# Optimization experiments

Hardware: AMD Instinct MI355X
Metric: run time of the kernel (lower is better)

The kernel has to match this reference:

```python
import jax, jax.numpy as jnp
import numpy as np

D, HEADS, HD, L, P, DFF = 256, 8, 32, 4, 4, 2048
B, NQ = 4, 900
SHAPES = [(128, 128), (64, 64), (32, 32), (16, 16)]
S = sum(h * w for h, w in SHAPES)


def setup_inputs():
    ks = iter(jax.random.split(jax.random.key(0), 20))
    rn = lambda *s: jax.random.normal(next(ks), s, jnp.float32) * 0.02
    cxcy = jax.random.uniform(next(ks), (B, NQ, 1, 2), minval=0.1, maxval=0.9)
    wh = jax.random.uniform(next(ks), (B, NQ, 1, 2), minval=0.05, maxval=0.3)
    ref = jnp.broadcast_to(jnp.concatenate([cxcy, wh], -1), (B, NQ, L, 4))
    starts = np.cumsum([0] + [h * w for h, w in SHAPES[:-1]])
    return dict(
        query=jax.random.normal(next(ks), (B, NQ, D), jnp.float32),
        query_pos=jax.random.normal(next(ks), (B, NQ, D), jnp.float32),
        reference_points=ref,
        input_flatten=jax.random.normal(next(ks), (B, S, D), jnp.float32),
        input_spatial_shapes=jnp.array(SHAPES, jnp.int32),
        input_level_start_index=jnp.array(starts, jnp.int32),
        sa_in_w=rn(3, D, D), sa_in_b=jnp.zeros((3, D)),
        sa_out_w=rn(D, D), sa_out_b=jnp.zeros((D,)),
        norm1_g=jnp.ones((D,)), norm1_b=jnp.zeros((D,)),
        value_w=rn(D, D), value_b=jnp.zeros((D,)),
        off_w=rn(D, HEADS * L * P * 2),
        off_b=jax.random.uniform(next(ks), (HEADS * L * P * 2,), minval=-1.0, maxval=1.0),
        aw_w=rn(D, HEADS * L * P), aw_b=jnp.zeros((HEADS * L * P,)),
        ca_out_w=rn(D, D), ca_out_b=jnp.zeros((D,)),
        norm2_g=jnp.ones((D,)), norm2_b=jnp.zeros((D,)),
        lin1_w=rn(D, DFF), lin1_b=jnp.zeros((DFF,)),
        lin2_w=rn(DFF, D), lin2_b=jnp.zeros((D,)),
        norm3_g=jnp.ones((D,)), norm3_b=jnp.zeros((D,)),
    )


def _ln(x, g, b, eps=1e-5):
    m = x.mean(-1, keepdims=True)
    v = ((x - m) ** 2).mean(-1, keepdims=True)
    return (x - m) * jax.lax.rsqrt(v + eps) * g + b


def _msdeform(q, input_flatten, ref, shapes, starts, value_w, value_b,
              off_w, off_b, aw_w, aw_b, out_w, out_b):
    Bq, Nq, _ = q.shape
    # value: (B, heads, S, head_dim)
    v = (input_flatten @ value_w + value_b).reshape(Bq, -1, HEADS, HD).transpose(0, 2, 1, 3)
    off = (q @ off_w + off_b).reshape(Bq, Nq, HEADS, L, P, 2).transpose(0, 2, 1, 3, 4, 5)
    aw = jax.nn.softmax((q @ aw_w + aw_b).reshape(Bq, Nq, HEADS, L * P), axis=-1)
    aw = aw.reshape(Bq, Nq, HEADS, L, P).transpose(0, 2, 1, 3, 4)  # (B,H,Nq,L,P)
    refc = ref[:, None, :, :, None, :]  # (B,1,Nq,L,1,4)
    # box refs: center + offset/P * wh * 0.5  (Deformable-DETR convention)
    loc = refc[..., :2] + off / P * refc[..., 2:] * 0.5  # (B,H,Nq,L,P,2)
    out = jnp.zeros((Bq, HEADS, Nq, HD), q.dtype)
    for l, (H, W) in enumerate(shapes):
        vl = jax.lax.dynamic_slice_in_dim(v, starts[l], H * W, axis=2)  # (B,H,HW,hd)
        x = loc[:, :, :, l, :, 0] * W - 0.5  # align_corners=False pixel coords
        y = loc[:, :, :, l, :, 1] * H - 0.5
        x0, y0 = jnp.floor(x), jnp.floor(y)
        dx, dy = x - x0, y - y0

        def g(xi, yi):
            valid = (xi >= 0) & (xi < W) & (yi >= 0) & (yi < H)  # zero padding
            idx = (jnp.clip(yi, 0, H - 1) * W + jnp.clip(xi, 0, W - 1)).astype(jnp.int32)
            gat = jnp.take_along_axis(vl, idx.reshape(Bq, HEADS, Nq * P, 1), axis=2)
            return gat.reshape(Bq, HEADS, Nq, P, HD) * valid[..., None]

        samp = (((1 - dx) * (1 - dy))[..., None] * g(x0, y0)
                + (dx * (1 - dy))[..., None] * g(x0 + 1, y0)
                + ((1 - dx) * dy)[..., None] * g(x0, y0 + 1)
                + (dx * dy)[..., None] * g(x0 + 1, y0 + 1))
        out = out + jnp.sum(aw[:, :, :, l, :, None] * samp, axis=3)
    return out.transpose(0, 2, 1, 3).reshape(Bq, Nq, D) @ out_w + out_b


def _layer(query, query_pos, reference_points, input_flatten, shapes, starts, p):
    Bq, Nq, _ = query.shape
    qk = query + query_pos
    heads = lambda x: x.reshape(Bq, Nq, HEADS, HD).transpose(0, 2, 1, 3)
    qh = heads(qk @ p['sa_in_w'][0] + p['sa_in_b'][0])
    kh = heads(qk @ p['sa_in_w'][1] + p['sa_in_b'][1])
    vh = heads(query @ p['sa_in_w'][2] + p['sa_in_b'][2])
    attn = jax.nn.softmax(jnp.einsum('bhqd,bhkd->bhqk', qh, kh) * (HD ** -0.5), axis=-1)
    sa = jnp.einsum('bhqk,bhkd->bhqd', attn, vh).transpose(0, 2, 1, 3).reshape(Bq, Nq, D)
    sa = sa @ p['sa_out_w'] + p['sa_out_b']
    x = _ln(query + sa, p['norm1_g'], p['norm1_b'])
    ca = _msdeform(x + query_pos, input_flatten, reference_points, shapes, starts,
                   p['value_w'], p['value_b'], p['off_w'], p['off_b'],
                   p['aw_w'], p['aw_b'], p['ca_out_w'], p['ca_out_b'])
    x = _ln(x + ca, p['norm2_g'], p['norm2_b'])
    ffn = jax.nn.relu(x @ p['lin1_w'] + p['lin1_b']) @ p['lin2_w'] + p['lin2_b']
    return _ln(x + ffn, p['norm3_g'], p['norm3_b'])


PNAMES = ['sa_in_w', 'sa_in_b', 'sa_out_w', 'sa_out_b', 'norm1_g', 'norm1_b',
          'value_w', 'value_b', 'off_w', 'off_b', 'aw_w', 'aw_b',
          'ca_out_w', 'ca_out_b', 'norm2_g', 'norm2_b',
          'lin1_w', 'lin1_b', 'lin2_w', 'lin2_b', 'norm3_g', 'norm3_b']


def reference(query, query_pos, reference_points, input_flatten,
              input_spatial_shapes, input_level_start_index,
              sa_in_w, sa_in_b, sa_out_w, sa_out_b, norm1_g, norm1_b,
              value_w, value_b, off_w, off_b, aw_w, aw_b,
              ca_out_w, ca_out_b, norm2_g, norm2_b,
              lin1_w, lin1_b, lin2_w, lin2_b, norm3_g, norm3_b):
    # spatial shapes / start indices are static structural metadata
    shapes = [(int(h), int(w)) for h, w in np.asarray(input_spatial_shapes)]
    starts = [int(s) for s in np.asarray(input_level_start_index)]
    p = dict(zip(PNAMES, (sa_in_w, sa_in_b, sa_out_w, sa_out_b, norm1_g, norm1_b,
                          value_w, value_b, off_w, off_b, aw_w, aw_b,
                          ca_out_w, ca_out_b, norm2_g, norm2_b,
                          lin1_w, lin1_b, lin2_w, lin2_b, norm3_g, norm3_b)))
    return _layer(query, query_pos, reference_points, input_flatten, shapes, starts, p)
```

## Files before the change

kernel.cpp:

```cpp
#include <hip/hip_runtime.h>
#include <hip/hip_bf16.h>

#define DD   256
#define NH   8
#define HDIM 32
#define LV   4
#define NP   4
#define DFF  2048
#define BB   4
#define NQQ  900
#define SS   21760

typedef __bf16 bf16x8 __attribute__((ext_vector_type(8)));
typedef __bf16 bf16x2 __attribute__((ext_vector_type(2)));
typedef float  f32x4  __attribute__((ext_vector_type(4)));

__device__ inline void stval(float* p, float v) { *p = v; }
__device__ inline void stval(__bf16* p, float v) { *p = (__bf16)v; }

__device__ __forceinline__ void gload16(const void* g, void* l) {
    __builtin_amdgcn_global_load_lds(
        (const __attribute__((address_space(1))) void*)g,
        (__attribute__((address_space(3))) void*)l, 16, 0, 0);
}

struct TPtrs {
    const float* s[10];
    __bf16* d[10];
};

__global__ void transp_all(TPtrs P) {
    const int Ks[10] = {256, 256, 256, 256, 256, 256, 256, 256, 256, 2048};
    const int Ns[10] = {256, 256, 256, 256, 256, 256, 128, 256, 2048, 256};
    const int tiles[10] = {64, 64, 64, 64, 64, 64, 32, 64, 512, 512};
    int t = blockIdx.x;
    int j = 0, base = 0;
    while (t >= base + tiles[j]) { base += tiles[j]; j++; }
    int lt = t - base;
    int K = Ks[j], N = Ns[j];
    int tn = N >> 5;
    int nb = (lt % tn) * 32, kb = (lt / tn) * 32;
    const float* W = P.s[j];
    __bf16* Wt = P.d[j];
    __shared__ float tbuf[32][33];
    for (int i = threadIdx.y; i < 32; i += 8)
        tbuf[i][threadIdx.x] = W[(size_t)(kb + i) * N + nb + threadIdx.x];
    __syncthreads();
    for (int i = threadIdx.y; i < 32; i += 8)
        Wt[(size_t)(nb + i) * K + kb + threadIdx.x] = (__bf16)tbuf[threadIdx.x][i];
}

#define BM 64
#define BN 64
#define BKK 64

template <typename AT, typename OT, int RELU, int NSUB, bool LNF>
__global__ __launch_bounds__(256) void mfma_gemm(
    const AT* __restrict__ A, const float* __restrict__ A2,
    const __bf16* __restrict__ Wt,
    const float* __restrict__ bias, const float* __restrict__ bias2, int nsplit,
    const float* __restrict__ res, const float* __restrict__ lng,
    const float* __restrict__ lnb,
    OT* __restrict__ C, int M, int N, int K) {
    int tid = threadIdx.x;
    int lane = tid & 63;
    int wave = tid >> 6;
    int wr = wave >> 1, wc = wave & 1;
    int m0 = blockIdx.y * BM;
    int n0 = blockIdx.x * (BN * NSUB);

    __shared__ __attribute__((aligned(16))) __bf16 As[BM * BKK];
    __shared__ __attribute__((aligned(16))) __bf16 Bs[NSUB][BN * BKK];
    __shared__ float rsum[LNF ? 64 : 1][2];
    __shared__ float rsum2[LNF ? 64 : 1][2];

    f32x4 acc[NSUB][2][2] = {};

    int srow = tid >> 2;
    int sq = tid & 3;
    int u0 = sq << 1;
    int p0 = (u0 ^ (srow & 7)) * 8;
    int p1 = ((u0 + 1) ^ (srow & 7)) * 8;
    int fr = lane & 15, gq = lane >> 4;

    for (int k0 = 0; k0 < K; k0 += BKK) {
        {
            int gm = m0 + srow;
            bf16x8 v0 = {}, v1 = {};
            if (gm < M) {
                if constexpr (sizeof(AT) == 4) {
                    const float* ap = (const float*)A + (size_t)gm * K + k0 + sq * 16;
                    f32x4 f0 = *(const f32x4*)(ap + 0);
                    f32x4 f1 = *(const f32x4*)(ap + 4);
                    f32x4 f2 = *(const f32x4*)(ap + 8);
                    f32x4 f3 = *(const f32x4*)(ap + 12);
                    if (A2) {
                        const float* ap2 = A2 + (size_t)gm * K + k0 + sq * 16;
                        f0 += *(const f32x4*)(ap2 + 0);
                        f1 += *(const f32x4*)(ap2 + 4);
                        f2 += *(const f32x4*)(ap2 + 8);
                        f3 += *(const f32x4*)(ap2 + 12);
                    }
#pragma unroll
                    for (int e = 0; e < 4; e++) {
                        v0[e] = (__bf16)f0[e]; v0[e + 4] = (__bf16)f1[e];
                        v1[e] = (__bf16)f2[e]; v1[e + 4] = (__bf16)f3[e];
                    }
                } else {
                    const __bf16* ap = (const __bf16*)A + (size_t)gm * K + k0 + sq * 16;
                    v0 = *(const bf16x8*)(ap);
                    v1 = *(const bf16x8*)(ap + 8);
                }
            }
            *(bf16x8*)(&As[srow * 64 + p0]) = v0;
            *(bf16x8*)(&As[srow * 64 + p1]) = v1;
        }
#pragma unroll
        for (int ns = 0; ns < NSUB; ns++) {
            int gn = n0 + ns * BN + srow;
            const __bf16* bp = Wt + (size_t)gn * K + k0 + sq * 16;
            bf16x8 w0 = *(const bf16x8*)(bp);
            bf16x8 w1 = *(const bf16x8*)(bp + 8);
            *(bf16x8*)(&Bs[ns][srow * 64 + p0]) = w0;
            *(bf16x8*)(&Bs[ns][srow * 64 + p1]) = w1;
        }
        __syncthreads();
#pragma unroll
        for (int ks = 0; ks < 2; ks++) {
            bf16x8 a[2];
#pragma unroll
            for (int i = 0; i < 2; i++) {
                int ma = wr * 32 + i * 16 + fr;
                a[i] = *(const bf16x8*)(&As[ma * 64 + ((ks * 4 + gq) ^ (ma & 7)) * 8]);
            }
#pragma unroll
            for (int ns = 0; ns < NSUB; ns++) {
                bf16x8 b[2];
#pragma unroll
                for (int j = 0; j < 2; j++) {
                    int nb = wc * 32 + j * 16 + fr;
                    b[j] = *(const bf16x8*)(&Bs[ns][nb * 64 + ((ks * 4 + gq) ^ (nb & 7)) * 8]);
                }
#pragma unroll
                for (int i = 0; i < 2; i++)
#pragma unroll
                    for (int j = 0; j < 2; j++)
                        acc[ns][i][j] = __builtin_amdgcn_mfma_f32_16x16x32_bf16(a[i], b[j], acc[ns][i][j], 0, 0, 0);
            }
        }
        __syncthreads();
    }
    int orow = gq * 4;
    if constexpr (!LNF) {
#pragma unroll
        for (int ns = 0; ns < NSUB; ns++)
#pragma unroll
            for (int i = 0; i < 2; i++)
#pragma unroll
                for (int j = 0; j < 2; j++) {
                    int gn = n0 + ns * BN + wc * 32 + j * 16 + fr;
                    float bv = (gn < nsplit) ? bias[gn] : bias2[gn - nsplit];
#pragma unroll
                    for (int r = 0; r < 4; r++) {
                        int gm = m0 + wr * 32 + i * 16 + orow + r;
                        if (gm < M) {
                            float v = acc[ns][i][j][r] + bv;
                            if (RELU) v = fmaxf(v, 0.f);
                            stval(C + (size_t)gm * N + gn, v);
                        }
                    }
                }
    } else {
        float part[2][4] = {};
#pragma unroll
        for (int ns = 0; ns < NSUB; ns++)
#pragma unroll
            for (int i = 0; i < 2; i++)
#pragma unroll
                for (int j = 0; j < 2; j++) {
                    int gn = ns * BN + wc * 32 + j * 16 + fr;
                    float bv = bias[gn];
#pragma unroll
                    for (int r = 0; r < 4; r++) {
                        int gm = m0 + wr * 32 + i * 16 + orow + r;
                        float rv = (gm < M) ? res[(size_t)gm * 256 + gn] : 0.f;
                        float x = acc[ns][i][j][r] + bv + rv;
                        acc[ns][i][j][r] = x;
                        part[i][r] += x;
                    }
                }
#pragma unroll
        for (int i = 0; i < 2; i++)
#pragma unroll
            for (int r = 0; r < 4; r++) {
                float v = part[i][r];
                v += __shfl_xor(v, 1);
                v += __shfl_xor(v, 2);
                v += __shfl_xor(v, 4);
                v += __shfl_xor(v, 8);
                part[i][r] = v;
            }
        if (fr == 0) {
#pragma unroll
            for (int i = 0; i < 2; i++)
#pragma unroll
                for (int r = 0; r < 4; r++)
                    rsum[wr * 32 + i * 16 + orow + r][wc] = part[i][r];
        }
        __syncthreads();
        float mean[2][4];
#pragma unroll
        for (int i = 0; i < 2; i++)
#pragma unroll
            for (int r = 0; r < 4; r++) {
                int rl = wr * 32 + i * 16 + orow + r;
                mean[i][r] = (rsum[rl][0] + rsum[rl][1]) * (1.f / 256.f);
            }
        float p2[2][4] = {};
#pragma unroll
        for (int ns = 0; ns < NSUB; ns++)
#pragma unroll
            for (int i = 0; i < 2; i++)
#pragma unroll
                for (int j = 0; j < 2; j++)
#pragma unroll
                    for (int r = 0; r < 4; r++) {
                        float d = acc[ns][i][j][r] - mean[i][r];
                        p2[i][r] += d * d;
                    }
#pragma unroll
        for (int i = 0; i < 2; i++)
#pragma unroll
            for (int r = 0; r < 4; r++) {
                float v = p2[i][r];
                v += __shfl_xor(v, 1);
                v += __shfl_xor(v, 2);
                v += __shfl_xor(v, 4);
                v += __shfl_xor(v, 8);
                p2[i][r] = v;
            }
        if (fr == 0) {
#pragma unroll
            for (int i = 0; i < 2; i++)
#pragma unroll
                for (int r = 0; r < 4; r++)
                    rsum2[wr * 32 + i * 16 + orow + r][wc] = p2[i][r];
        }
        __syncthreads();
        float rstd[2][4];
#pragma unroll
        for (int i = 0; i < 2; i++)
#pragma unroll
            for (int r = 0; r < 4; r++) {
                int rl = wr * 32 + i * 16 + orow + r;
                float var = (rsum2[rl][0] + rsum2[rl][1]) * (1.f / 256.f);
                rstd[i][r] = rsqrtf(var + 1e-5f);
            }
#pragma unroll
        for (int ns = 0; ns < NSUB; ns++)
#pragma unroll
            for (int i = 0; i < 2; i++)
#pragma unroll
                for (int j = 0; j < 2; j++) {
                    int gn = ns * BN + wc * 32 + j * 16 + fr;
                    float gv = lng[gn], bev = lnb[gn];
#pragma unroll
                    for (int r = 0; r < 4; r++) {
                        int gm = m0 + wr * 32 + i * 16 + orow + r;
                        if (gm < M) {
                            float y = (acc[ns][i][j][r] - mean[i][r]) * rstd[i][r] * gv + bev;
                            stval(C + (size_t)gm * 256 + gn, y);
                        }
                    }
                }
    }
}

__global__ __launch_bounds__(256) void value_gemm4(
    const float* __restrict__ A, const __bf16* __restrict__ Wt,
    const float* __restrict__ bias, __bf16* __restrict__ C) {
    int tid = threadIdx.x;
    int lane = tid & 63;
    int wave = tid >> 6;
    int fr = lane & 15, gq = lane >> 4;
    int m0 = blockIdx.x * 64;

    __shared__ __attribute__((aligned(16))) __bf16 As[2][64 * 64];
    __shared__ __attribute__((aligned(16))) __bf16 Bq[2][4][64 * 64];

    f32x4 acc[4][4] = {};

    int srow = tid >> 2;
    int sq = tid & 3;
    int u0 = sq << 1;
    int p0 = (u0 ^ (srow & 7)) * 8;
    int p1 = ((u0 + 1) ^ (srow & 7)) * 8;

    int c_row = lane >> 3;
    int c_u = lane & 7;
    int gu = c_u ^ c_row;
    const __bf16* bsrc0 = Wt + (size_t)(wave * 64 + c_row) * 256 + gu * 8;
    const float* aptr = A + (size_t)(m0 + srow) * 256 + sq * 16;

    f32x4 fa0 = *(const f32x4*)(aptr + 0);
    f32x4 fa1 = *(const f32x4*)(aptr + 4);
    f32x4 fa2 = *(const f32x4*)(aptr + 8);
    f32x4 fa3 = *(const f32x4*)(aptr + 12);
    __builtin_amdgcn_sched_barrier(0);
#pragma unroll
    for (int c = 0; c < 8; c++)
        gload16(bsrc0 + (size_t)c * 8 * 256, &Bq[0][wave][c * 512]);
    asm volatile("s_waitcnt vmcnt(8)" ::: "memory");
    __builtin_amdgcn_sched_barrier(0);
    {
        bf16x8 v0, v1;
#pragma unroll
        for (int e = 0; e < 4; e++) {
            v0[e] = (__bf16)fa0[e]; v0[e + 4] = (__bf16)fa1[e];
            v1[e] = (__bf16)fa2[e]; v1[e + 4] = (__bf16)fa3[e];
        }
        *(bf16x8*)(&As[0][srow * 64 + p0]) = v0;
        *(bf16x8*)(&As[0][srow * 64 + p1]) = v1;
    }
    asm volatile("s_waitcnt lgkmcnt(0)" ::: "memory");
    __builtin_amdgcn_s_barrier();

#pragma unroll
    for (int step = 0; step < 4; step++) {
        int p = step & 1;
        if (step < 3) {
            const float* ap2 = aptr + (step + 1) * 64;
            fa0 = *(const f32x4*)(ap2 + 0);
            fa1 = *(const f32x4*)(ap2 + 4);
            fa2 = *(const f32x4*)(ap2 + 8);
            fa3 = *(const f32x4*)(ap2 + 12);
            __builtin_amdgcn_sched_barrier(0);
            const __bf16* bsrc = bsrc0 + (step + 1) * 64;
#pragma unroll
            for (int c = 0; c < 8; c++)
                gload16(bsrc + (size_t)c * 8 * 256, &Bq[p ^ 1][wave][c * 512]);
            asm volatile("s_waitcnt vmcnt(12)" ::: "memory");
        } else {
            asm volatile("s_waitcnt vmcnt(0)" ::: "memory");
        }
        __builtin_amdgcn_sched_barrier(0);
#pragma unroll
        for (int ks = 0; ks < 2; ks++) {
            bf16x8 a[4], b[4];
#pragma unroll
            for (int i = 0; i < 4; i++) {
                int ma = i * 16 + fr;
                a[i] = *(const bf16x8*)(&As[p][ma * 64 + ((ks * 4 + gq) ^ (ma & 7)) * 8]);
                b[i] = *(const bf16x8*)(&Bq[p][wave][ma * 64 + ((ks * 4 + gq) ^ (ma & 7)) * 8]);
            }
#pragma unroll
            for (int i = 0; i < 4; i++)
#pragma unroll
                for (int j = 0; j < 4; j++)
                    acc[i][j] = __builtin_amdgcn_mfma_f32_16x16x32_bf16(a[i], b[j], acc[i][j], 0, 0, 0);
        }
        if (step < 3) {
            asm volatile("s_waitcnt vmcnt(8)" ::: "memory");
            __builtin_amdgcn_sched_barrier(0);
            bf16x8 v0, v1;
#pragma unroll
            for (int e = 0; e < 4; e++) {
                v0[e] = (__bf16)fa0[e]; v0[e + 4] = (__bf16)fa1[e];
                v1[e] = (__bf16)fa2[e]; v1[e + 4] = (__bf16)fa3[e];
            }
            *(bf16x8*)(&As[p ^ 1][srow * 64 + p0]) = v0;
            *(bf16x8*)(&As[p ^ 1][srow * 64 + p1]) = v1;
            asm volatile("s_waitcnt lgkmcnt(0)" ::: "memory");
            __builtin_amdgcn_s_barrier();
        }
    }

#pragma unroll
    for (int i = 0; i < 4; i++)
#pragma unroll
        for (int j = 0; j < 4; j++) {
            int gn = wave * 64 + j * 16 + fr;
            float bv = bias[gn];
#pragma unroll
            for (int r = 0; r < 4; r++) {
                int gm = m0 + i * 16 + gq * 4 + r;
                C[(size_t)gm * 256 + gn] = (__bf16)(acc[i][j][r] + bv);
            }
        }
}

__global__ void fillmark(float* o, int n, float v) {
    int i = blockIdx.x * blockDim.x + threadIdx.x;
    if (i < n) o[i] = v;
}

__global__ void ln_res(const float* a, const float* b,
                       const float* g, const float* be, float* o) {
    int row = blockIdx.x;
    int t = threadIdx.x;
    float x = a[(size_t)row * DD + t] + b[(size_t)row * DD + t];
    __shared__ float red[DD];
    red[t] = x;
    __syncthreads();
    for (int s = 128; s > 0; s >>= 1) {
        if (t < s) red[t] += red[t + s];
        __syncthreads();
    }
    float m = red[0] * (1.f / DD);
    __syncthreads();
    float d0 = x - m;
    red[t] = d0 * d0;
    __syncthreads();
    for (int s = 128; s > 0; s >>= 1) {
        if (t < s) red[t] += red[t + s];
        __syncthreads();
    }
    float v = red[0] * (1.f / DD);
    o[(size_t)row * DD + t] = d0 * rsqrtf(v + 1e-5f) * g[t] + be[t];
}

#define QT 64
#define KT 64
#define NT ((NQQ + KT - 1) / KT)
#define QKLD 512

__global__ __launch_bounds__(256) void sa_attn_mfma(
    const __bf16* __restrict__ QK, const __bf16* __restrict__ V,
    float* __restrict__ O) {
    int blk = blockIdx.x;
    int tq = blk % NT;
    int bh = blk / NT;
    int h = bh % NH;
    int b = bh / NH;
    int tid = threadIdx.x;
    int lane = tid & 63;
    int wave = tid >> 6;
    int fr = lane & 15, gq = lane >> 4;
    int q0 = tq * QT;

    __shared__ __attribute__((aligned(16))) __bf16 Ks[KT][56];
    __shared__ __attribute__((aligned(16))) __bf16 Vt[HDIM][72];
    __shared__ __attribute__((aligned(16))) __bf16 Ps[4][16][72];

    int qrow = q0 + wave * 16 + fr;
    bf16x8 aq = {};
    if (qrow < NQQ)
        aq = *(const bf16x8*)(QK + ((size_t)(b * NQQ + qrow)) * QKLD + h * HDIM + gq * 8);

    f32x4 o0 = {}, o1 = {};
    float m_r[4] = {-1e30f, -1e30f, -1e30f, -1e30f};
    float l_r[4] = {0.f, 0.f, 0.f, 0.f};
    const float scale = 0.17677669529663687f;

    for (int kt = 0; kt < NT; kt++) {
        int kv0 = kt * KT;
        {
            int r = tid >> 2;
            int c8 = (tid & 3) * 8;
            int kvr = kv0 + r;
            bf16x8 kv_ = {}, vv_ = {};
            if (kvr < NQQ) {
                kv_ = *(const bf16x8*)(QK + ((size_t)(b * NQQ + kvr)) * QKLD + 256 + h * HDIM + c8);
                vv_ = *(const bf16x8*)(V + ((size_t)(b * NQQ + kvr)) * DD + h * HDIM + c8);
            }
            *(bf16x8*)(&Ks[r][c8]) = kv_;
#pragma unroll
            for (int j = 0; j < 8; j++) Vt[c8 + j][r] = vv_[j];
        }
        __syncthreads();

        f32x4 s[4];
#pragma unroll
        for (int f = 0; f < 4; f++) {
            bf16x8 bk = *(const bf16x8*)(&Ks[f * 16 + fr][gq * 8]);
            f32x4 z = {};
            s[f] = __builtin_amdgcn_mfma_f32_16x16x32_bf16(aq, bk, z, 0, 0, 0);
        }
#pragma unroll
        for (int f = 0; f < 4; f++) {
            bool valid = (kv0 + f * 16 + fr) < NQQ;
#pragma unroll
            for (int r = 0; r < 4; r++)
                s[f][r] = valid ? s[f][r] * scale : -1e30f;
        }
        float sc_[4];
#pragma unroll
        for (int r = 0; r < 4; r++) {
            float v = fmaxf(fmaxf(s[0][r], s[1][r]), fmaxf(s[2][r], s[3][r]));
            v = fmaxf(v, __shfl_xor(v, 1));
            v = fmaxf(v, __shfl_xor(v, 2));
            v = fmaxf(v, __shfl_xor(v, 4));
            v = fmaxf(v, __shfl_xor(v, 8));
            float mn = fmaxf(m_r[r], v);
            sc_[r] = expf(m_r[r] - mn);
            m_r[r] = mn;
        }
        float rs[4] = {0.f, 0.f, 0.f, 0.f};
#pragma unroll
        for (int f = 0; f < 4; f++)
#pragma unroll
            for (int r = 0; r < 4; r++) {
                float e = expf(s[f][r] - m_r[r]);
                s[f][r] = e;
                rs[r] += e;
            }
#pragma unroll
        for (int r = 0; r < 4; r++) {
            float v = rs[r];
            v += __shfl_xor(v, 1);
            v += __shfl_xor(v, 2);
            v += __shfl_xor(v, 4);
            v += __shfl_xor(v, 8);
            l_r[r] = l_r[r] * sc_[r] + v;
            o0[r] *= sc_[r];
            o1[r] *= sc_[r];
        }
#pragma unroll
        for (int f = 0; f < 4; f++)
#pragma unroll
            for (int r = 0; r < 4; r++)
                Ps[wave][gq * 4 + r][f * 16 + fr] = (__bf16)s[f][r];
#pragma unroll
        for (int c = 0; c < 2; c++) {
            bf16x8 ap = *(const bf16x8*)(&Ps[wave][fr][c * 32 + gq * 8]);
            bf16x8 bv0 = *(const bf16x8*)(&Vt[fr][c * 32 + gq * 8]);
            bf16x8 bv1 = *(const bf16x8*)(&Vt[16 + fr][c * 32 + gq * 8]);
            o0 = __builtin_amdgcn_mfma_f32_16x16x32_bf16(ap, bv0, o0, 0, 0, 0);
            o1 = __builtin_amdgcn_mfma_f32_16x16x32_bf16(ap, bv1, o1, 0, 0, 0);
        }
        __syncthreads();
    }
#pragma unroll
    for (int r = 0; r < 4; r++) {
        int qr = q0 + wave * 16 + gq * 4 + r;
        if (qr < NQQ) {
            float inv = 1.f / l_r[r];
            O[((size_t)(b * NQQ + qr)) * DD + h * HDIM + fr] = o0[r] * inv;
            O[((size_t)(b * NQQ + qr)) * DD + h * HDIM + 16 + fr] = o1[r] * inv;
        }
    }
}

#define OAW 384

__global__ __launch_bounds__(256) void msdeform3(
    const __bf16* __restrict__ val, const __bf16* __restrict__ oa,
    const float* __restrict__ ref, float* __restrict__ out) {
    int tid = threadIdx.x;
    int row = blockIdx.x;
    int b_ = row / NQQ;

    __shared__ float sx[128], sy[128], sw[128];

    if (tid < 128) {
        int h = tid >> 4;
        int lp = tid & 15;
        int l = lp >> 2;
        float logit = (float)oa[(size_t)row * OAW + 256 + h * 16 + lp];
        float ox = (float)oa[(size_t)row * OAW + h * 32 + lp * 2];
        float oy = (float)oa[(size_t)row * OAW + h * 32 + lp * 2 + 1];
        const float* rp = ref + ((size_t)row * LV + l) * 4;
        float cx = rp[0], cy = rp[1], rw = rp[2], rh = rp[3];
        float mv = logit;
        mv = fmaxf(mv, __shfl_xor(mv, 1));
        mv = fmaxf(mv, __shfl_xor(mv, 2));
        mv = fmaxf(mv, __shfl_xor(mv, 4));
        mv = fmaxf(mv, __shfl_xor(mv, 8));
        float e = expf(logit - mv);
        float sum = e;
        sum += __shfl_xor(sum, 1);
        sum += __shfl_xor(sum, 2);
        sum += __shfl_xor(sum, 4);
        sum += __shfl_xor(sum, 8);
        int Wl = 128 >> l;
        float lx = cx + ox * (1.0f / NP) * rw * 0.5f;
        float ly = cy + oy * (1.0f / NP) * rh * 0.5f;
        sx[tid] = lx * Wl - 0.5f;
        sy[tid] = ly * Wl - 0.5f;
        sw[tid] = e / sum;
    }
    __syncthreads();

    int cpar = tid & 7;
    int dgrp = (tid >> 3) & 3;
    int h = tid >> 5;
    const int stt[4] = {0, 16384, 20480, 21504};
    const __bf16* vb = val + (size_t)b_ * SS * DD + h * HDIM + dgrp * 8;
    float facc[8] = {};
#pragma unroll
    for (int k = 0; k < 8; k++) {
        int combo = cpar * 8 + k;
        int lp = combo >> 2;
        int tap = combo & 3;
        int l = lp >> 2;
        int Wl = 128 >> l;
        int cidx = h * 16 + lp;
        float x = sx[cidx], y = sy[cidx], w = sw[cidx];
        float x0f = floorf(x), y0f = floorf(y);
        float dx = x - x0f, dy = y - y0f;
        int xi = (int)x0f + (tap & 1);
        int yi = (int)y0f + (tap >> 1);
        float wt = ((tap & 1) ? dx : 1.f - dx) * ((tap >> 1) ? dy : 1.f - dy) * w;
        if ((xi >= 0) & (xi < Wl) & (yi >= 0) & (yi < Wl)) {
            bf16x8 t = *(const bf16x8*)(vb + (size_t)(stt[l] + yi * Wl + xi) * DD);
#pragma unroll
            for (int e = 0; e < 8; e++) facc[e] += wt * (float)t[e];
        }
    }
#pragma unroll
    for (int e = 0; e < 8; e++) {
        facc[e] += __shfl_xor(facc[e], 1);
        facc[e] += __shfl_xor(facc[e], 2);
        facc[e] += __shfl_xor(facc[e], 4);
    }
    float v = facc[0];
#pragma unroll
    for (int e = 1; e < 8; e++) if (cpar == e) v = facc[e];
    out[(size_t)row * DD + tid] = v;
}

extern "C" void kernel_launch(void* const* d_in, const int* in_sizes, int n_in,
                              void* d_out, int out_size, void* d_ws, size_t ws_size,
                              hipStream_t stream) {
    const float* query      = (const float*)d_in[0];
    const float* query_pos  = (const float*)d_in[1];
    const float* refpts     = (const float*)d_in[2];
    const float* input_flat = (const float*)d_in[3];
    const float* sa_in_w    = (const float*)d_in[6];
    const float* sa_in_b    = (const float*)d_in[7];
    const float* sa_out_w   = (const float*)d_in[8];
    const float* sa_out_b   = (const float*)d_in[9];
    const float* norm1_g    = (const float*)d_in[10];
    const float* norm1_b    = (const float*)d_in[11];
    const float* value_w    = (const float*)d_in[12];
    const float* value_b    = (const float*)d_in[13];
    const float* off_w      = (const float*)d_in[14];
    const float* off_b      = (const float*)d_in[15];
    const float* aw_w       = (const float*)d_in[16];
    const float* aw_b       = (const float*)d_in[17];
    const float* ca_out_w   = (const float*)d_in[18];
    const float* ca_out_b   = (const float*)d_in[19];
    const float* norm2_g    = (const float*)d_in[20];
    const float* norm2_b    = (const float*)d_in[21];
    const float* lin1_w     = (const float*)d_in[22];
    const float* lin1_b     = (const float*)d_in[23];
    const float* lin2_w     = (const float*)d_in[24];
    const float* lin2_b     = (const float*)d_in[25];
    const float* norm3_g    = (const float*)d_in[26];
    const float* norm3_b    = (const float*)d_in[27];
    float* out = (float*)d_out;

    const int M = BB * NQQ;
    const int NE = M * DD;
    const size_t slotBytes = (size_t)NE * 4;
    const size_t wElems = 6 * 65536 + 32768 + 65536 + 2 * 524288;
    const size_t wBytes = wElems * 2;
    const size_t bigBytes = (size_t)BB * SS * DD * 2;
    const size_t needBytes = 3 * slotBytes + wBytes + bigBytes;
    if (ws_size < needBytes) {
        float mark = 1000.0f + (float)(ws_size >> 20);
        fillmark<<<(out_size + 255) / 256, 256, 0, stream>>>(out, out_size, mark);
        return;
    }

    char* wsb = (char*)d_ws;
    float* s0 = (float*)(wsb);
    float* s1 = (float*)(wsb + slotBytes);
    float* s2 = (float*)(wsb + 2 * slotBytes);
    __bf16* wb = (__bf16*)(wsb + 3 * slotBytes);
    __bf16* vbig = (__bf16*)(wsb + 3 * slotBytes + wBytes);

    __bf16* wt_q   = wb;
    __bf16* wt_k   = wb + 65536;
    __bf16* wt_v   = wb + 131072;
    __bf16* wt_sa  = wb + 196608;
    __bf16* wt_val = wb + 262144;
    __bf16* wt_off = wb + 327680;
    __bf16* wt_aw  = wb + 393216;
    __bf16* wt_ca  = wb + 425984;
    __bf16* wt_l1  = wb + 491520;
    __bf16* wt_l2  = wb + 1015808;

    TPtrs tp;
    tp.s[0] = sa_in_w;          tp.d[0] = wt_q;
    tp.s[1] = sa_in_w + 65536;  tp.d[1] = wt_k;
    tp.s[2] = sa_in_w + 131072; tp.d[2] = wt_v;
    tp.s[3] = sa_out_w;         tp.d[3] = wt_sa;
    tp.s[4] = value_w;          tp.d[4] = wt_val;
    tp.s[5] = off_w;            tp.d[5] = wt_off;
    tp.s[6] = aw_w;             tp.d[6] = wt_aw;
    tp.s[7] = ca_out_w;         tp.d[7] = wt_ca;
    tp.s[8] = lin1_w;           tp.d[8] = wt_l1;
    tp.s[9] = lin2_w;           tp.d[9] = wt_l2;
    transp_all<<<1504, dim3(32, 8), 0, stream>>>(tp);

    __bf16* qkbuf = (__bf16*)s1;
    __bf16* Vp = (__bf16*)s2;
    __bf16* oabuf = (__bf16*)s1;

    const int mt = (M + BM - 1) / BM;
    const int BIG = 1 << 30;

    mfma_gemm<float, __bf16, 0, 2, false><<<dim3(4, mt), 256, 0, stream>>>(
        query, query_pos, wt_q, sa_in_b, sa_in_b, BIG,
        nullptr, nullptr, nullptr, qkbuf, M, 512, DD);
    mfma_gemm<float, __bf16, 0, 1, false><<<dim3(4, mt), 256, 0, stream>>>(
        query, nullptr, wt_v, sa_in_b + 512, sa_in_b, BIG,
        nullptr, nullptr, nullptr, Vp, M, DD, DD);
    sa_attn_mfma<<<BB * NH * NT, 256, 0, stream>>>(qkbuf, Vp, s0);
    mfma_gemm<float, float, 0, 4, true><<<dim3(1, mt), 256, 0, stream>>>(
        s0, nullptr, wt_sa, sa_out_b, sa_out_b, BIG,
        query, norm1_g, norm1_b, s2, M, DD, DD);
    value_gemm4<<<(BB * SS) / 64, 256, 0, stream>>>(input_flat, wt_val, value_b, vbig);
    mfma_gemm<float, __bf16, 0, 1, false><<<dim3(6, mt), 256, 0, stream>>>(
        s2, query_pos, wt_off, off_b, aw_b, 256,
        nullptr, nullptr, nullptr, oabuf, M, OAW, DD);
    msdeform3<<<M, 256, 0, stream>>>(vbig, oabuf, refpts, s0);
    mfma_gemm<float, float, 0, 4, true><<<dim3(1, mt), 256, 0, stream>>>(
        s0, nullptr, wt_ca, ca_out_b, ca_out_b, BIG,
        s2, norm2_g, norm2_b, s1, M, DD, DD);
    mfma_gemm<float, __bf16, 1, 2, false><<<dim3(16, mt), 256, 0, stream>>>(
        s1, nullptr, wt_l1, lin1_b, lin1_b, BIG,
        nullptr, nullptr, nullptr, vbig, M, DFF, DD);
    mfma_gemm<__bf16, float, 0, 1, false><<<dim3(4, mt), 256, 0, stream>>>(
        vbig, nullptr, wt_l2, lin2_b, lin2_b, BIG,
        nullptr, nullptr, nullptr, s0, M, DD, DFF);
    ln_res<<<M, DD, 0, stream>>>(s1, s0, norm3_g, norm3_b, out);
}
```

Measured before the change: 212.9 us.

## Fuse value projection and self-attention QKV GEMMs into one heterogeneous launch

Merges the large value-projection GEMM and the Q/K and V self-attention projection GEMMs into one kernel. Each block picks its sub-task from its block index, and all three share one dynamically carved LDS buffer. The intent is to remove two launches and let the small QKV GEMMs fill CUs alongside the large value GEMM instead of running serially. In exchange, every block reserves the maximum LDS (80KB), which may reduce occupancy for the smaller GEMM blocks.

```diff
diff --git a/kernel.cpp b/kernel.cpp
--- a/kernel.cpp
+++ b/kernel.cpp
@@ -55,7 +55,8 @@
 #define BKK 64
 
 template <typename AT, typename OT, int RELU, int NSUB, bool LNF>
-__global__ __launch_bounds__(256) void mfma_gemm(
+__device__ __forceinline__ void gemm_body(
+    int bx, int by, char* ldsraw,
     const AT* __restrict__ A, const float* __restrict__ A2,
     const __bf16* __restrict__ Wt,
     const float* __restrict__ bias, const float* __restrict__ bias2, int nsplit,
@@ -66,13 +67,13 @@
     int lane = tid & 63;
     int wave = tid >> 6;
     int wr = wave >> 1, wc = wave & 1;
-    int m0 = blockIdx.y * BM;
-    int n0 = blockIdx.x * (BN * NSUB);
-
-    __shared__ __attribute__((aligned(16))) __bf16 As[BM * BKK];
-    __shared__ __attribute__((aligned(16))) __bf16 Bs[NSUB][BN * BKK];
-    __shared__ float rsum[LNF ? 64 : 1][2];
-    __shared__ float rsum2[LNF ? 64 : 1][2];
+    int m0 = by * BM;
+    int n0 = bx * (BN * NSUB);
+
+    __bf16* As = (__bf16*)ldsraw;
+    __bf16* Bs = (__bf16*)(ldsraw + BM * BKK * 2);
+    float* rsum  = (float*)(ldsraw + BM * BKK * 2 + NSUB * BN * BKK * 2);
+    float* rsum2 = rsum + 128;
 
     f32x4 acc[NSUB][2][2] = {};
 
@@ -121,8 +122,8 @@
             const __bf16* bp = Wt + (size_t)gn * K + k0 + sq * 16;
             bf16x8 w0 = *(const bf16x8*)(bp);
             bf16x8 w1 = *(const bf16x8*)(bp + 8);
-            *(bf16x8*)(&Bs[ns][srow * 64 + p0]) = w0;
-            *(bf16x8*)(&Bs[ns][srow * 64 + p1]) = w1;
+            *(bf16x8*)(&Bs[ns * BN * BKK + srow * 64 + p0]) = w0;
+            *(bf16x8*)(&Bs[ns * BN * BKK + srow * 64 + p1]) = w1;
         }
         __syncthreads();
 #pragma unroll
@@ -139,7 +140,7 @@
 #pragma unroll
                 for (int j = 0; j < 2; j++) {
                     int nb = wc * 32 + j * 16 + fr;
-                    b[j] = *(const bf16x8*)(&Bs[ns][nb * 64 + ((ks * 4 + gq) ^ (nb & 7)) * 8]);
+                    b[j] = *(const bf16x8*)(&Bs[ns * BN * BKK + nb * 64 + ((ks * 4 + gq) ^ (nb & 7)) * 8]);
                 }
 #pragma unroll
                 for (int i = 0; i < 2; i++)
@@ -205,7 +206,7 @@
             for (int i = 0; i < 2; i++)
 #pragma unroll
                 for (int r = 0; r < 4; r++)
-                    rsum[wr * 32 + i * 16 + orow + r][wc] = part[i][r];
+                    rsum[(wr * 32 + i * 16 + orow + r) * 2 + wc] = part[i][r];
         }
         __syncthreads();
         float mean[2][4];
@@ -214,7 +215,7 @@
 #pragma unroll
             for (int r = 0; r < 4; r++) {
                 int rl = wr * 32 + i * 16 + orow + r;
-                mean[i][r] = (rsum[rl][0] + rsum[rl][1]) * (1.f / 256.f);
+                mean[i][r] = (rsum[rl * 2] + rsum[rl * 2 + 1]) * (1.f / 256.f);
             }
         float p2[2][4] = {};
 #pragma unroll
@@ -244,7 +245,7 @@
             for (int i = 0; i < 2; i++)
 #pragma unroll
                 for (int r = 0; r < 4; r++)
-                    rsum2[wr * 32 + i * 16 + orow + r][wc] = p2[i][r];
+                    rsum2[(wr * 32 + i * 16 + orow + r) * 2 + wc] = p2[i][r];
         }
         __syncthreads();
         float rstd[2][4];
@@ -253,7 +254,7 @@
 #pragma unroll
             for (int r = 0; r < 4; r++) {
                 int rl = wr * 32 + i * 16 + orow + r;
-                float var = (rsum2[rl][0] + rsum2[rl][1]) * (1.f / 256.f);
+                float var = (rsum2[rl * 2] + rsum2[rl * 2 + 1]) * (1.f / 256.f);
                 rstd[i][r] = rsqrtf(var + 1e-5f);
             }
 #pragma unroll
@@ -276,17 +277,31 @@
     }
 }
 
-__global__ __launch_bounds__(256) void value_gemm4(
+template <typename AT, typename OT, int RELU, int NSUB, bool LNF>
+__global__ __launch_bounds__(256) void mfma_gemm(
+    const AT* __restrict__ A, const float* __restrict__ A2,
+    const __bf16* __restrict__ Wt,
+    const float* __restrict__ bias, const float* __restrict__ bias2, int nsplit,
+    const float* __restrict__ res, const float* __restrict__ lng,
+    const float* __restrict__ lnb,
+    OT* __restrict__ C, int M, int N, int K) {
+    __shared__ __attribute__((aligned(16))) char lds[BM * BKK * 2 + NSUB * BN * BKK * 2 + (LNF ? 1024 : 0)];
+    gemm_body<AT, OT, RELU, NSUB, LNF>(blockIdx.x, blockIdx.y, lds, A, A2, Wt,
+                                       bias, bias2, nsplit, res, lng, lnb, C, M, N, K);
+}
+
+__device__ __forceinline__ void value_body(
+    int bx, char* ldsraw,
     const float* __restrict__ A, const __bf16* __restrict__ Wt,
     const float* __restrict__ bias, __bf16* __restrict__ C) {
     int tid = threadIdx.x;
     int lane = tid & 63;
     int wave = tid >> 6;
     int fr = lane & 15, gq = lane >> 4;
-    int m0 = blockIdx.x * 64;
-
-    __shared__ __attribute__((aligned(16))) __bf16 As[2][64 * 64];
-    __shared__ __attribute__((aligned(16))) __bf16 Bq[2][4][64 * 64];
+    int m0 = bx * 64;
+
+    __bf16* As = (__bf16*)ldsraw;
+    __bf16* Bq = (__bf16*)(ldsraw + 16384);
 
     f32x4 acc[4][4] = {};
 
@@ -309,7 +324,7 @@
     __builtin_amdgcn_sched_barrier(0);
 #pragma unroll
     for (int c = 0; c < 8; c++)
-        gload16(bsrc0 + (size_t)c * 8 * 256, &Bq[0][wave][c * 512]);
+        gload16(bsrc0 + (size_t)c * 8 * 256, &Bq[wave * 4096 + c * 512]);
     asm volatile("s_waitcnt vmcnt(8)" ::: "memory");
     __builtin_amdgcn_sched_barrier(0);
     {
@@ -319,8 +334,8 @@
             v0[e] = (__bf16)fa0[e]; v0[e + 4] = (__bf16)fa1[e];
             v1[e] = (__bf16)fa2[e]; v1[e + 4] = (__bf16)fa3[e];
         }
-        *(bf16x8*)(&As[0][srow * 64 + p0]) = v0;
-        *(bf16x8*)(&As[0][srow * 64 + p1]) = v1;
+        *(bf16x8*)(&As[srow * 64 + p0]) = v0;
+        *(bf16x8*)(&As[srow * 64 + p1]) = v1;
     }
     asm volatile("s_waitcnt lgkmcnt(0)" ::: "memory");
     __builtin_amdgcn_s_barrier();
@@ -338,7 +353,7 @@
             const __bf16* bsrc = bsrc0 + (step + 1) * 64;
 #pragma unroll
             for (int c = 0; c < 8; c++)
-                gload16(bsrc + (size_t)c * 8 * 256, &Bq[p ^ 1][wave][c * 512]);
+                gload16(bsrc + (size_t)c * 8 * 256, &Bq[((p ^ 1) * 4 + wave) * 4096 + c * 512]);
             asm volatile("s_waitcnt vmcnt(12)" ::: "memory");
         } else {
             asm volatile("s_waitcnt vmcnt(0)" ::: "memory");
@@ -350,8 +365,8 @@
 #pragma unroll
             for (int i = 0; i < 4; i++) {
                 int ma = i * 16 + fr;
-                a[i] = *(const bf16x8*)(&As[p][ma * 64 + ((ks * 4 + gq) ^ (ma & 7)) * 8]);
-                b[i] = *(const bf16x8*)(&Bq[p][wave][ma * 64 + ((ks * 4 + gq) ^ (ma & 7)) * 8]);
+                a[i] = *(const bf16x8*)(&As[p * 4096 + ma * 64 + ((ks * 4 + gq) ^ (ma & 7)) * 8]);
+                b[i] = *(const bf16x8*)(&Bq[(p * 4 + wave) * 4096 + ma * 64 + ((ks * 4 + gq) ^ (ma & 7)) * 8]);
             }
 #pragma unroll
             for (int i = 0; i < 4; i++)
@@ -368,8 +383,8 @@
                 v0[e] = (__bf16)fa0[e]; v0[e + 4] = (__bf16)fa1[e];
                 v1[e] = (__bf16)fa2[e]; v1[e + 4] = (__bf16)fa3[e];
             }
-            *(bf16x8*)(&As[p ^ 1][srow * 64 + p0]) = v0;
-            *(bf16x8*)(&As[p ^ 1][srow * 64 + p1]) = v1;
+            *(bf16x8*)(&As[(p ^ 1) * 4096 + srow * 64 + p0]) = v0;
+            *(bf16x8*)(&As[(p ^ 1) * 4096 + srow * 64 + p1]) = v1;
             asm volatile("s_waitcnt lgkmcnt(0)" ::: "memory");
             __builtin_amdgcn_s_barrier();
         }
@@ -387,6 +402,34 @@
                 C[(size_t)gm * 256 + gn] = (__bf16)(acc[i][j][r] + bv);
             }
         }
+}
+
+#define NVALB 1360
+#define NQKB  228
+#define NVB   228
+
+__global__ __launch_bounds__(256) void fused_head(
+    const float* __restrict__ input_flat, const __bf16* __restrict__ wt_val,
+    const float* __restrict__ value_b, __bf16* __restrict__ vbig,
+    const float* __restrict__ query, const float* __restrict__ query_pos,
+    const __bf16* __restrict__ wt_q, const float* __restrict__ sa_in_b,
+    __bf16* __restrict__ qkbuf, const __bf16* __restrict__ wt_v,
+    __bf16* __restrict__ Vp, int M) {
+    __shared__ __attribute__((aligned(16))) char lds[81920];
+    int bx = blockIdx.x;
+    if (bx < NVALB) {
+        value_body(bx, lds, input_flat, wt_val, value_b, vbig);
+    } else if (bx < NVALB + NQKB) {
+        int b2 = bx - NVALB;
+        gemm_body<float, __bf16, 0, 2, false>(b2 & 3, b2 >> 2, lds,
+            query, query_pos, wt_q, sa_in_b, sa_in_b, 1 << 30,
+            nullptr, nullptr, nullptr, qkbuf, M, 512, 256);
+    } else {
+        int b2 = bx - NVALB - NQKB;
+        gemm_body<float, __bf16, 0, 1, false>(b2 & 3, b2 >> 2, lds,
+            query, nullptr, wt_v, sa_in_b + 512, sa_in_b, 1 << 30,
+            nullptr, nullptr, nullptr, Vp, M, 256, 256);
+    }
 }
 
 __global__ void fillmark(float* o, int n, float v) {
@@ -701,17 +744,13 @@
     const int mt = (M + BM - 1) / BM;
     const int BIG = 1 << 30;
 
-    mfma_gemm<float, __bf16, 0, 2, false><<<dim3(4, mt), 256, 0, stream>>>(
-        query, query_pos, wt_q, sa_in_b, sa_in_b, BIG,
-        nullptr, nullptr, nullptr, qkbuf, M, 512, DD);
-    mfma_gemm<float, __bf16, 0, 1, false><<<dim3(4, mt), 256, 0, stream>>>(
-        query, nullptr, wt_v, sa_in_b + 512, sa_in_b, BIG,
-        nullptr, nullptr, nullptr, Vp, M, DD, DD);
+    fused_head<<<NVALB + NQKB + NVB, 256, 0, stream>>>(
+        input_flat, wt_val, value_b, vbig,
+        query, query_pos, wt_q, sa_in_b, qkbuf, wt_v, Vp, M);
     sa_attn_mfma<<<BB * NH * NT, 256, 0, stream>>>(qkbuf, Vp, s0);
     mfma_gemm<float, float, 0, 4, true><<<dim3(1, mt), 256, 0, stream>>>(
         s0, nullptr, wt_sa, sa_out_b, sa_out_b, BIG,
         query, norm1_g, norm1_b, s2, M, DD, DD);
-    value_gemm4<<<(BB * SS) / 64, 256, 0, stream>>>(input_flat, wt_val, value_b, vbig);
     mfma_gemm<float, __bf16, 0, 1, false><<<dim3(6, mt), 256, 0, stream>>>(
         s2, query_pos, wt_off, off_b, aw_b, 256,
         nullptr, nullptr, nullptr, oabuf, M, OAW, DD);
```

Result: faster. 203.8 us (-4.3%).
